# Kernel tuning notes

Measured on AMD Instinct MI355X. Metric: run time of the kernel, lower is better.

The kernel has to match this reference:

```python
import jax, jax.numpy as jnp
import numpy as np

UNITS = 1024
EMBED = 512
K = 32000
HIDDEN_LAYERS = 2
BATCH = 64
SEQ = 256
ALPHA = 0.2  # leaky_relu slope


def _leaky_relu(z):
    return jnp.where(z > 0, z, ALPHA * z)


def setup_inputs() -> dict:
    key = jax.random.key(0)
    ks = jax.random.split(key, 10)
    s_in = 1.0 / np.sqrt(UNITS)
    s_e = 1.0 / np.sqrt(EMBED)
    return {
        "x": jax.random.randint(ks[0], (BATCH, SEQ), 0, K),
        "x_embedding": jax.random.normal(ks[1], (K, EMBED), dtype=jnp.float32) * 0.05,
        "w_y": jax.random.normal(ks[2], (UNITS, UNITS), dtype=jnp.float32) * s_in,
        "w_x": jax.random.normal(ks[3], (EMBED, UNITS), dtype=jnp.float32) * s_e,
        "b_in": jax.random.uniform(ks[4], (UNITS,), dtype=jnp.float32, minval=-0.05, maxval=0.05),
        "w_hidden": jax.random.normal(ks[5], (HIDDEN_LAYERS, UNITS, UNITS), dtype=jnp.float32) * s_in,
        "b_hidden": jax.random.uniform(ks[6], (HIDDEN_LAYERS, UNITS), dtype=jnp.float32, minval=-0.05, maxval=0.05),
        "w_out": jax.random.normal(ks[7], (UNITS, UNITS), dtype=jnp.float32) * s_in,
        "b_out": jax.random.uniform(ks[8], (UNITS,), dtype=jnp.float32, minval=-0.05, maxval=0.05),
        "h0": jax.random.uniform(ks[9], (1, UNITS), dtype=jnp.float32, minval=-0.05, maxval=0.05),
    }


def reference(x, x_embedding, w_y, w_x, b_in, w_hidden, b_hidden, w_out, b_out, h0):
    n = x.shape[0]
    # Gather all embeddings up front: [n, T, E] -> time-major [T, n, E]
    xe_all = jnp.swapaxes(x_embedding[x], 0, 1)

    def step(y0, xe):
        # MLPUnit: sum of input projections + bias, inner activation
        h = _leaky_relu(y0 @ w_y + xe @ w_x + b_in)

        def layer(hc, wb):
            w, bb = wb
            return _leaky_relu(hc @ w + bb), None

        h, _ = jax.lax.scan(layer, h, (w_hidden, b_hidden))
        y1 = y0 + (h @ w_out + b_out)  # highway residual
        return y1, y1

    y0 = jnp.broadcast_to(h0, (n, h0.shape[1]))
    _, yr = jax.lax.scan(step, y0, xe_all)  # [T, n, units]
    return jnp.swapaxes(yr, 0, 1)  # [n, T, units]
```

## Files before the change

kernel.cpp:

```cpp
#include <hip/hip_runtime.h>


constexpr int B = 64, T = 256, U = 1024, E = 512;
constexpr int BU = B * U;
constexpr int APITCH = 1156;
constexpr int RPITCH = 264;
constexpr int WOPITCH = 9;

#define LRELU(v) ((v) > 0.f ? (v) : 0.2f * (v))

using f4 = float __attribute__((ext_vector_type(4)));

__device__ __forceinline__ void llc_store(float* p, float v) {
  __hip_atomic_store(p, v, __ATOMIC_RELAXED, __HIP_MEMORY_SCOPE_AGENT);
}
__device__ __forceinline__ unsigned llc_flag(const unsigned* p) {
  return __hip_atomic_load(p, __ATOMIC_RELAXED, __HIP_MEMORY_SCOPE_AGENT);
}
__device__ __forceinline__ void llc_post(unsigned* p, unsigned v) {
  __hip_atomic_store(p, v, __ATOMIC_RELAXED, __HIP_MEMORY_SCOPE_AGENT);
}

#define COMPUTE_ACC(WB)                                          \
  do {                                                           \
    _Pragma("unroll") for (int r = 0; r < 8; ++r) acc[r] =       \
        (f4){0.f, 0.f, 0.f, 0.f};                                \
    _Pragma("unroll") for (int q = 0; q < 4; ++q) {              \
      const f4 w0 = WB[4 * q], w1 = WB[4 * q + 1];               \
      const f4 w2 = WB[4 * q + 2], w3 = WB[4 * q + 3];           \
      const int ab = abase_k + 4 * q;                            \
      _Pragma("unroll") for (int r = 0; r < 8; ++r) {            \
        f4 a = *(const f4*)&a_s[r * APITCH + ab];                \
        acc[r] += a.x * w0 + a.y * w1 + a.z * w2 + a.w * w3;     \
      }                                                          \
    }                                                            \
  } while (0)

__global__ void k_init(unsigned* __restrict__ flags) {
  int tid = blockIdx.x * 256 + threadIdx.x;
  if (tid < 512) flags[tid] = 0u;
}

__global__ __launch_bounds__(256) void k_xproj(
    const int* __restrict__ x, const float* __restrict__ emb,
    const float* __restrict__ w_x, const float* __restrict__ b_in,
    float* __restrict__ xp) {
  __shared__ float a_s[64][36];
  __shared__ float w_s[32][64];
  __shared__ int idxs[64];
  const int tid = threadIdx.x;
  const int m0 = blockIdx.x * 64;
  const int c0 = blockIdx.y * 64;
  if (tid < 64) {
    int m = m0 + tid;
    idxs[tid] = x[(m & 63) * T + (m >> 6)];
  }
  __syncthreads();
  const int rq = tid >> 4, cq = tid & 15;
  float acc[4][4] = {};
  for (int k0 = 0; k0 < E; k0 += 32) {
#pragma unroll
    for (int rep = 0; rep < 8; ++rep) {
      int e = rep * 256 + tid;
      int r = e >> 5, k = e & 31;
      a_s[r][k] = emb[(size_t)idxs[r] * E + k0 + k];
    }
#pragma unroll
    for (int rep = 0; rep < 2; ++rep) {
      int e = rep * 256 + tid;
      int kr = e >> 4, q = e & 15;
      *(float4*)&w_s[kr][4 * q] =
          *(const float4*)(w_x + (size_t)(k0 + kr) * U + c0 + 4 * q);
    }
    __syncthreads();
#pragma unroll
    for (int kc = 0; kc < 32; kc += 4) {
      float4 a4[4], w4[4];
#pragma unroll
      for (int i = 0; i < 4; ++i) a4[i] = *(const float4*)&a_s[4 * rq + i][kc];
#pragma unroll
      for (int kk = 0; kk < 4; ++kk)
        w4[kk] = *(const float4*)&w_s[kc + kk][4 * cq];
#pragma unroll
      for (int i = 0; i < 4; ++i) {
        const float av[4] = {a4[i].x, a4[i].y, a4[i].z, a4[i].w};
#pragma unroll
        for (int kk = 0; kk < 4; ++kk) {
          acc[i][0] += av[kk] * w4[kk].x;
          acc[i][1] += av[kk] * w4[kk].y;
          acc[i][2] += av[kk] * w4[kk].z;
          acc[i][3] += av[kk] * w4[kk].w;
        }
      }
    }
    __syncthreads();
  }
  const float4 bb = *(const float4*)(b_in + c0 + 4 * cq);
  const float bv[4] = {bb.x, bb.y, bb.z, bb.w};
#pragma unroll
  for (int i = 0; i < 4; ++i) {
    float4 o;
    o.x = acc[i][0] + bv[0];
    o.y = acc[i][1] + bv[1];
    o.z = acc[i][2] + bv[2];
    o.w = acc[i][3] + bv[3];
    *(float4*)(xp + (size_t)(m0 + 4 * rq + i) * U + c0 + 4 * cq) = o;
  }
}

__global__ __launch_bounds__(512, 2) void k_seq(
    const float* __restrict__ xp, const float* __restrict__ w_y,
    const float* __restrict__ w_h, const float* __restrict__ b_h,
    const float* __restrict__ w_out, const float* __restrict__ b_out,
    const float* __restrict__ h0, float* __restrict__ out,
    float* __restrict__ slots, unsigned* __restrict__ flags) {
  __shared__ float a_s[8 * APITCH];
  __shared__ float red2[64 * RPITCH];
  __shared__ float c2_s[32], u0_s[32];
  const int tid = threadIdx.x;
  const int bid = blockIdx.x;
  const int cg = ((bid & 7) << 2) | ((bid >> 3) & 3);
  const int rg = bid >> 5;
  const int w = tid >> 6, l = tid & 63;
  const int ci = l & 7;
  const int sp = w * 8 + (l >> 3);
  const int cb = 4 * ci, k0 = 16 * sp;
  const int abase_k = 36 * (sp >> 1) + 16 * (sp & 1);
  const int frow = 8 * rg + (tid >> 5);
  const int fu = 32 * cg + (tid & 31);
  const int srow = l >> 3, scol = l & 7;

  float* const wos = red2;
  float* const wys = a_s;
  f4 w2reg[16];
#pragma unroll
  for (int jj = 0; jj < 16; ++jj) w2reg[jj] = (f4){0.f, 0.f, 0.f, 0.f};
  f4 c2a = (f4){0.f, 0.f, 0.f, 0.f}, u0a = (f4){0.f, 0.f, 0.f, 0.f};
  {
    f4 nx0, nx1, nx2, nx3, nwy;
    {
      const float* wo = w_out + (size_t)tid * U;
      nx0 = *(const f4*)wo;
      nx1 = *(const f4*)(wo + 4);
      const float* wo2 = w_out + (size_t)(tid + 512) * U;
      nx2 = *(const f4*)wo2;
      nx3 = *(const f4*)(wo2 + 4);
      if (tid < 64)
        nwy = *(const f4*)(w_y + (size_t)(tid >> 3) * U + 32 * cg +
                           4 * (tid & 7));
    }
    for (int mi = 0; mi < 128; ++mi) {
      const int m0 = mi * 8;
#pragma unroll
      for (int q = 0; q < 4; ++q) {
        wos[tid * WOPITCH + q] = nx0[q];
        wos[tid * WOPITCH + 4 + q] = nx1[q];
        wos[(tid + 512) * WOPITCH + q] = nx2[q];
        wos[(tid + 512) * WOPITCH + 4 + q] = nx3[q];
      }
      if (tid < 64) *(f4*)&wys[(tid >> 3) * 36 + 4 * (tid & 7)] = nwy;
      __syncthreads();
      if (mi < 127) {
        const int m1 = m0 + 8;
        const float* wo = w_out + (size_t)tid * U + m1;
        nx0 = *(const f4*)wo;
        nx1 = *(const f4*)(wo + 4);
        const float* wo2 = w_out + (size_t)(tid + 512) * U + m1;
        nx2 = *(const f4*)wo2;
        nx3 = *(const f4*)(wo2 + 4);
        if (tid < 64)
          nwy = *(const f4*)(w_y + (size_t)(m1 + (tid >> 3)) * U + 32 * cg +
                             4 * (tid & 7));
      }
#pragma unroll
      for (int mm = 0; mm < 8; ++mm) {
        const f4 wy = *(const f4*)&wys[mm * 36 + cb];
#pragma unroll
        for (int jj = 0; jj < 16; ++jj)
          w2reg[jj] += wos[(16 * sp + jj) * WOPITCH + mm] * wy;
        if (tid < 8) {
          c2a += b_out[m0 + mm] * wy;
          u0a += h0[m0 + mm] * wy;
        }
      }
      __syncthreads();
    }
  }
  if (tid < 8) {
    *(f4*)&c2_s[cb] = c2a;
    *(f4*)&u0_s[cb] = u0a;
  }
  __syncthreads();
  float u_reg = 0.f, y_reg = 0.f, c2_lane = 0.f;
  if (tid < 256) {
    c2_lane = c2_s[tid & 31];
    u_reg = u0_s[tid & 31];
    y_reg = h0[fu];
    float h1 = LRELU(u_reg + xp[(size_t)frow * U + fu]);
    llc_store(slots + (size_t)frow * U + fu, h1);
  }
  asm volatile("" ::: "memory");
  __builtin_amdgcn_s_waitcnt(0);
  __syncthreads();
  if (tid == 0) llc_post(&flags[rg * 32 + cg], 1u);

  f4 wreg[16];
  {
    const float* wp = w_h + (size_t)k0 * U + 32 * cg + cb;
#pragma unroll
    for (int jj = 0; jj < 16; ++jj)
      wreg[jj] = *(const f4*)(wp + (size_t)jj * U);
  }

  for (int Q = 1; Q <= 3 * T; ++Q) {
    const int j = (Q - 1) % 3, t = (Q - 1) / 3;
    const float* Asrc =
        slots + (size_t)((Q + 1) & 1) * BU + (size_t)(8 * rg) * U;
    float* slotw = slots + (size_t)(Q & 1) * BU;
    float preA = 0.f, preB = 0.f;
    if (tid < 256) {
      if (j == 0)
        preA = b_h[fu];
      else if (j == 1)
        preA = b_h[U + fu];
      else {
        if (t < T - 1) preA = xp[((size_t)(t + 1) * B + frow) * U + fu];
        preB = b_out[fu];
      }
    }
    {
      f4 sv0, sv1, sv2, sv3;
      int sd0, sd1, sd2, sd3;
#define STAGE_SLAB(I, SV, SD)                                              \
      {                                                                    \
        const int pc = ((w << 2) + I + cg) & 31;                           \
        const unsigned* fp = &flags[rg * 32 + pc];                         \
        while (!__all(llc_flag(fp) >= (unsigned)Q))                        \
          __builtin_amdgcn_s_sleep(1);                                     \
        asm volatile("" ::: "memory");                                     \
        const float* pb =                                                  \
            Asrc + (size_t)srow * U + (size_t)(32 * pc + 4 * scol);        \
        asm volatile("global_load_dwordx4 %0, %1, off sc1"                 \
                     : "=v"(SV)                                            \
                     : "v"(pb));                                           \
        SD = srow * APITCH + 36 * pc + 4 * scol;                           \
      }
      STAGE_SLAB(0, sv0, sd0)
      STAGE_SLAB(1, sv1, sd1)
      STAGE_SLAB(2, sv2, sd2)
      STAGE_SLAB(3, sv3, sd3)
#undef STAGE_SLAB
      asm volatile("s_waitcnt vmcnt(0)" ::: "memory");
      *(f4*)&a_s[sd0] = sv0;
      *(f4*)&a_s[sd1] = sv1;
      *(f4*)&a_s[sd2] = sv2;
      *(f4*)&a_s[sd3] = sv3;
    }
    __syncthreads();
    f4 acc[8];
    if (j == 2)
      COMPUTE_ACC(w2reg);
    else
      COMPUTE_ACC(wreg);
#pragma unroll
    for (int r = 0; r < 8; ++r)
      *(f4*)&red2[sp * RPITCH + r * 32 + cb] = acc[r];
    __syncthreads();
    if (tid < 256) {
      float s0 = 0.f, s1 = 0.f, s2 = 0.f, s3 = 0.f;
#pragma unroll
      for (int z = 0; z < 64; z += 4) {
        s0 += red2[(z + 0) * RPITCH + tid];
        s1 += red2[(z + 1) * RPITCH + tid];
        s2 += red2[(z + 2) * RPITCH + tid];
        s3 += red2[(z + 3) * RPITCH + tid];
      }
      const float sum = (s0 + s1) + (s2 + s3);
      const size_t yi = (size_t)frow * U + fu;
      if (j < 2) {
        llc_store(slotw + yi, LRELU(sum + preA));
      } else {
        u_reg += sum + c2_lane;
        llc_store(slotw + yi, LRELU(u_reg + preA));
      }
    }
    asm volatile("" ::: "memory");
    __builtin_amdgcn_s_waitcnt(0);
    __syncthreads();
    if (tid == 0) llc_post(&flags[rg * 32 + cg], (unsigned)(Q + 1));
    if (j == 2) {
      f4 acc2[8];
      {
        f4* acc = acc2;
        if (true) COMPUTE_ACC(wreg);
      }
#pragma unroll
      for (int r = 0; r < 8; ++r)
        *(f4*)&red2[sp * RPITCH + r * 32 + cb] = acc2[r];
      __syncthreads();
      if (tid < 256) {
        float s0 = 0.f, s1 = 0.f, s2 = 0.f, s3 = 0.f;
#pragma unroll
        for (int z = 0; z < 64; z += 4) {
          s0 += red2[(z + 0) * RPITCH + tid];
          s1 += red2[(z + 1) * RPITCH + tid];
          s2 += red2[(z + 2) * RPITCH + tid];
          s3 += red2[(z + 3) * RPITCH + tid];
        }
        y_reg += (s0 + s1) + (s2 + s3) + preB;
        out[((size_t)frow * T + t) * U + fu] = y_reg;
      }
    }
    if (Q < 3 * T) {
      const float* Wn = (j == 0)   ? (w_h + (size_t)U * U)
                        : (j == 1) ? w_out
                                   : w_h;
      const float* wp = Wn + (size_t)k0 * U + 32 * cg + cb;
#pragma unroll
      for (int jj = 0; jj < 16; ++jj)
        wreg[jj] = *(const f4*)(wp + (size_t)jj * U);
    }
  }
}

extern "C" void kernel_launch(void* const* d_in, const int* in_sizes, int n_in,
                              void* d_out, int out_size, void* d_ws,
                              size_t ws_size, hipStream_t stream) {
  const int* x = (const int*)d_in[0];
  const float* emb = (const float*)d_in[1];
  const float* w_y = (const float*)d_in[2];
  const float* w_x = (const float*)d_in[3];
  const float* b_in = (const float*)d_in[4];
  const float* w_h = (const float*)d_in[5];
  const float* b_h = (const float*)d_in[6];
  const float* w_out = (const float*)d_in[7];
  const float* b_out = (const float*)d_in[8];
  const float* h0 = (const float*)d_in[9];
  float* out = (float*)d_out;

  float* ws = (float*)d_ws;
  float* xpb = ws;
  float* slots = xpb + (size_t)T * B * U;
  float* dead = slots + 2 * (size_t)BU;
  unsigned* flags = (unsigned*)(dead + (size_t)BU);

  k_init<<<2, 256, 0, stream>>>(flags);
  dim3 g1(256, 16);
  k_xproj<<<g1, 256, 0, stream>>>(x, emb, w_x, b_in, xpb);

  void* args[] = {&xpb,   &w_y, &w_h, &b_h,   &w_out,
                  &b_out, &h0,  &out, &slots, &flags};
  hipLaunchCooperativeKernel((void*)k_seq, dim3(256), dim3(512), args, 0u,
                             stream);
}
```

Measured before the change: 5.237 ms.

## Fuse output GEMV into recurrent step, shuffle-reduce partials, drop staging barrier

Each wave now stages and consumes only its own K-slice of activations, so the __syncthreads before compute is removed. The wave reads flags for just the four producer blocks it depends on. Partial sums are reduced inside the wave with xor-shuffles, which shrinks the LDS reduction from 64 rows to 8. The y-output GEMV for the highway residual is computed in the same pass as the u-update (dual accumulators), and the upper 256 threads finalise it. This removes a second compute/reduce/barrier phase per timestep, at the cost of extra register pressure from the dual accumulators.

Result: slower. 7.387 ms (+41.0%).

```diff
diff --git a/kernel.cpp b/kernel.cpp
--- a/kernel.cpp
+++ b/kernel.cpp
@@ -23,8 +23,6 @@
 
 #define COMPUTE_ACC(WB)                                          \
   do {                                                           \
-    _Pragma("unroll") for (int r = 0; r < 8; ++r) acc[r] =       \
-        (f4){0.f, 0.f, 0.f, 0.f};                                \
     _Pragma("unroll") for (int q = 0; q < 4; ++q) {              \
       const f4 w0 = WB[4 * q], w1 = WB[4 * q + 1];               \
       const f4 w2 = WB[4 * q + 2], w3 = WB[4 * q + 3];           \
@@ -32,6 +30,33 @@
       _Pragma("unroll") for (int r = 0; r < 8; ++r) {            \
         f4 a = *(const f4*)&a_s[r * APITCH + ab];                \
         acc[r] += a.x * w0 + a.y * w1 + a.z * w2 + a.w * w3;     \
+      }                                                          \
+    }                                                            \
+  } while (0)
+#define COMPUTE_DUAL(WBM, WBY)                                   \
+  do {                                                           \
+    _Pragma("unroll") for (int q = 0; q < 4; ++q) {              \
+      const f4 m0 = WBM[4 * q], m1 = WBM[4 * q + 1];             \
+      const f4 m2 = WBM[4 * q + 2], m3 = WBM[4 * q + 3];         \
+      const f4 y0 = WBY[4 * q], y1 = WBY[4 * q + 1];             \
+      const f4 y2 = WBY[4 * q + 2], y3 = WBY[4 * q + 3];         \
+      const int ab = abase_k + 4 * q;                            \
+      _Pragma("unroll") for (int r = 0; r < 8; ++r) {            \
+        f4 a = *(const f4*)&a_s[r * APITCH + ab];                \
+        acc[r] += a.x * m0 + a.y * m1 + a.z * m2 + a.w * m3;     \
+        accY[r] += a.x * y0 + a.y * y1 + a.z * y2 + a.w * y3;    \
+      }                                                          \
+    }                                                            \
+  } while (0)
+#define WAVE_REDUCE(ACC)                                         \
+  do {                                                           \
+    _Pragma("unroll") for (int r = 0; r < 8; ++r) {              \
+      _Pragma("unroll") for (int c = 0; c < 4; ++c) {            \
+        float v = ACC[r][c];                                     \
+        v += __shfl_xor(v, 8, 64);                               \
+        v += __shfl_xor(v, 16, 64);                              \
+        v += __shfl_xor(v, 32, 64);                              \
+        ACC[r][c] = v;                                           \
       }                                                          \
     }                                                            \
   } while (0)
@@ -115,7 +140,8 @@
     const float* __restrict__ h0, float* __restrict__ out,
     float* __restrict__ slots, unsigned* __restrict__ flags) {
   __shared__ float a_s[8 * APITCH];
-  __shared__ float red2[64 * RPITCH];
+  __shared__ float red_u[8 * RPITCH];
+  __shared__ float red_y[8 * RPITCH];
   __shared__ float c2_s[32], u0_s[32];
   const int tid = threadIdx.x;
   const int bid = blockIdx.x;
@@ -123,15 +149,19 @@
   const int rg = bid >> 5;
   const int w = tid >> 6, l = tid & 63;
   const int ci = l & 7;
-  const int sp = w * 8 + (l >> 3);
+  const int wq = (w + cg) & 7;
+  const int sp = 8 * wq + (l >> 3);
   const int cb = 4 * ci, k0 = 16 * sp;
   const int abase_k = 36 * (sp >> 1) + 16 * (sp & 1);
   const int frow = 8 * rg + (tid >> 5);
   const int fu = 32 * cg + (tid & 31);
-  const int srow = l >> 3, scol = l & 7;
-
-  float* const wos = red2;
-  float* const wys = a_s;
+  const int ro2 = tid - 256;
+  const int frow2 = 8 * rg + (ro2 >> 5);
+  const int fu2 = 32 * cg + (ro2 & 31);
+  const int srow = l >> 3;
+
+  float* const wos = a_s;
+  float* const wys = red_u;
   f4 w2reg[16];
 #pragma unroll
   for (int jj = 0; jj < 16; ++jj) w2reg[jj] = (f4){0.f, 0.f, 0.f, 0.f};
@@ -195,9 +225,10 @@
   if (tid < 256) {
     c2_lane = c2_s[tid & 31];
     u_reg = u0_s[tid & 31];
-    y_reg = h0[fu];
     float h1 = LRELU(u_reg + xp[(size_t)frow * U + fu]);
     llc_store(slots + (size_t)frow * U + fu, h1);
+  } else {
+    y_reg = h0[fu2];
   }
   asm volatile("" ::: "memory");
   __builtin_amdgcn_s_waitcnt(0);
@@ -223,58 +254,59 @@
         preA = b_h[fu];
       else if (j == 1)
         preA = b_h[U + fu];
-      else {
-        if (t < T - 1) preA = xp[((size_t)(t + 1) * B + frow) * U + fu];
-        preB = b_out[fu];
-      }
+      else if (t < T - 1)
+        preA = xp[((size_t)(t + 1) * B + frow) * U + fu];
+    } else if (j == 2) {
+      preB = b_out[fu2];
     }
     {
-      f4 sv0, sv1, sv2, sv3;
-      int sd0, sd1, sd2, sd3;
-#define STAGE_SLAB(I, SV, SD)                                              \
-      {                                                                    \
-        const int pc = ((w << 2) + I + cg) & 31;                           \
-        const unsigned* fp = &flags[rg * 32 + pc];                         \
-        while (!__all(llc_flag(fp) >= (unsigned)Q))                        \
-          __builtin_amdgcn_s_sleep(1);                                     \
-        asm volatile("" ::: "memory");                                     \
-        const float* pb =                                                  \
-            Asrc + (size_t)srow * U + (size_t)(32 * pc + 4 * scol);        \
-        asm volatile("global_load_dwordx4 %0, %1, off sc1"                 \
-                     : "=v"(SV)                                            \
-                     : "v"(pb));                                           \
-        SD = srow * APITCH + 36 * pc + 4 * scol;                           \
-      }
-      STAGE_SLAB(0, sv0, sd0)
-      STAGE_SLAB(1, sv1, sd1)
-      STAGE_SLAB(2, sv2, sd2)
-      STAGE_SLAB(3, sv3, sd3)
-#undef STAGE_SLAB
+      const unsigned* fp = &flags[rg * 32 + 4 * wq + (l & 3)];
+      while (!__all(llc_flag(fp) >= (unsigned)Q)) __builtin_amdgcn_s_sleep(1);
+    }
+    asm volatile("" ::: "memory");
+    {
+      const float* pb = Asrc + (size_t)srow * U + 128 * wq + cb;
+      f4 s0, s1, s2, s3;
+      asm volatile("global_load_dwordx4 %0, %1, off sc1"
+                   : "=v"(s0) : "v"(pb));
+      asm volatile("global_load_dwordx4 %0, %1, off sc1"
+                   : "=v"(s1) : "v"(pb + 32));
+      asm volatile("global_load_dwordx4 %0, %1, off sc1"
+                   : "=v"(s2) : "v"(pb + 64));
+      asm volatile("global_load_dwordx4 %0, %1, off sc1"
+                   : "=v"(s3) : "v"(pb + 96));
       asm volatile("s_waitcnt vmcnt(0)" ::: "memory");
-      *(f4*)&a_s[sd0] = sv0;
-      *(f4*)&a_s[sd1] = sv1;
-      *(f4*)&a_s[sd2] = sv2;
-      *(f4*)&a_s[sd3] = sv3;
-    }
-    __syncthreads();
-    f4 acc[8];
+      const int db = srow * APITCH + 144 * wq + cb;
+      *(f4*)&a_s[db] = s0;
+      *(f4*)&a_s[db + 36] = s1;
+      *(f4*)&a_s[db + 72] = s2;
+      *(f4*)&a_s[db + 108] = s3;
+    }
+    f4 acc[8], accY[8];
+#pragma unroll
+    for (int r = 0; r < 8; ++r) acc[r] = accY[r] = (f4){0.f, 0.f, 0.f, 0.f};
     if (j == 2)
-      COMPUTE_ACC(w2reg);
+      COMPUTE_DUAL(w2reg, wreg);
     else
       COMPUTE_ACC(wreg);
-#pragma unroll
-    for (int r = 0; r < 8; ++r)
-      *(f4*)&red2[sp * RPITCH + r * 32 + cb] = acc[r];
+    WAVE_REDUCE(acc);
+    if (j == 2) WAVE_REDUCE(accY);
+    if (l < 8) {
+#pragma unroll
+      for (int r = 0; r < 8; ++r)
+        *(f4*)&red_u[w * RPITCH + r * 32 + 4 * l] = acc[r];
+      if (j == 2) {
+#pragma unroll
+        for (int r = 0; r < 8; ++r)
+          *(f4*)&red_y[w * RPITCH + r * 32 + 4 * l] = accY[r];
+      }
+    }
     __syncthreads();
     if (tid < 256) {
-      float s0 = 0.f, s1 = 0.f, s2 = 0.f, s3 = 0.f;
-#pragma unroll
-      for (int z = 0; z < 64; z += 4) {
-        s0 += red2[(z + 0) * RPITCH + tid];
-        s1 += red2[(z + 1) * RPITCH + tid];
-        s2 += red2[(z + 2) * RPITCH + tid];
-        s3 += red2[(z + 3) * RPITCH + tid];
-      }
+      float s0 = red_u[0 * RPITCH + tid] + red_u[1 * RPITCH + tid];
+      float s1 = red_u[2 * RPITCH + tid] + red_u[3 * RPITCH + tid];
+      float s2 = red_u[4 * RPITCH + tid] + red_u[5 * RPITCH + tid];
+      float s3 = red_u[6 * RPITCH + tid] + red_u[7 * RPITCH + tid];
       const float sum = (s0 + s1) + (s2 + s3);
       const size_t yi = (size_t)frow * U + fu;
       if (j < 2) {
@@ -283,34 +315,18 @@
         u_reg += sum + c2_lane;
         llc_store(slotw + yi, LRELU(u_reg + preA));
       }
+    } else if (j == 2) {
+      float s0 = red_y[0 * RPITCH + ro2] + red_y[1 * RPITCH + ro2];
+      float s1 = red_y[2 * RPITCH + ro2] + red_y[3 * RPITCH + ro2];
+      float s2 = red_y[4 * RPITCH + ro2] + red_y[5 * RPITCH + ro2];
+      float s3 = red_y[6 * RPITCH + ro2] + red_y[7 * RPITCH + ro2];
+      y_reg += (s0 + s1) + (s2 + s3) + preB;
     }
     asm volatile("" ::: "memory");
     __builtin_amdgcn_s_waitcnt(0);
     __syncthreads();
     if (tid == 0) llc_post(&flags[rg * 32 + cg], (unsigned)(Q + 1));
-    if (j == 2) {
-      f4 acc2[8];
-      {
-        f4* acc = acc2;
-        if (true) COMPUTE_ACC(wreg);
-      }
-#pragma unroll
-      for (int r = 0; r < 8; ++r)
-        *(f4*)&red2[sp * RPITCH + r * 32 + cb] = acc2[r];
-      __syncthreads();
-      if (tid < 256) {
-        float s0 = 0.f, s1 = 0.f, s2 = 0.f, s3 = 0.f;
-#pragma unroll
-        for (int z = 0; z < 64; z += 4) {
-          s0 += red2[(z + 0) * RPITCH + tid];
-          s1 += red2[(z + 1) * RPITCH + tid];
-          s2 += red2[(z + 2) * RPITCH + tid];
-          s3 += red2[(z + 3) * RPITCH + tid];
-        }
-        y_reg += (s0 + s1) + (s2 + s3) + preB;
-        out[((size_t)frow * T + t) * U + fu] = y_reg;
-      }
-    }
+    if (j == 2 && tid >= 256) out[((size_t)frow2 * T + t) * U + fu2] = y_reg;
     if (Q < 3 * T) {
       const float* Wn = (j == 0)   ? (w_h + (size_t)U * U)
                         : (j == 1) ? w_out
```
